# Optimization experiments

Hardware: AMD Instinct MI355X
Metric: run time of the kernel (lower is better)

The kernel has to match this reference:

```python
import jax, jax.numpy as jnp
import numpy as np

NUM_TAGS = 32            # init arg
N = NUM_TAGS + 2         # internal num_tags (start/end appended)
START = N - 2
END = N - 1
B = 1024
T = 1024
NEG = -6969.0            # module's 'minus infinity' constant


def setup_inputs() -> dict:
    key = jax.random.key(0)
    k1, k2 = jax.random.split(key)
    features = jax.random.normal(k1, (B, T, N), dtype=jnp.float32)
    # learned parameter: transition matrix [N, N]
    transitions = jax.random.normal(k2, (N, N), dtype=jnp.float32)
    return {"features": features, "transitions": transitions}


def _viterbi(features, transitions):
    # features: [B, T, N]; transitions: [N, N]
    Bn, Tn, Nn = features.shape
    init = jnp.full((Bn, Nn), NEG, dtype=features.dtype).at[:, START].set(0.0)

    def step(scores, feat):
        # score[b, j, k] = scores[b, k] + feat[b, j] + transitions[j, k]
        sc = scores[:, None, :] + feat[:, :, None] + transitions[None, :, :]
        return jnp.max(sc, axis=-1), jnp.argmax(sc, axis=-1)

    feats_t = jnp.swapaxes(features, 0, 1)            # [T, B, N]
    scores, paths = jax.lax.scan(step, init, feats_t)  # paths: [T, B, N] int

    scores = scores + transitions[END]                # add transition to end tag
    best = jnp.max(scores, axis=-1)                   # [B]
    idx = jnp.argmax(scores, axis=-1)                 # [B]

    # backtrack through backpointers, from t = T-1 down to 0
    def back(i, path):
        ni = jnp.take_along_axis(path, i[:, None], axis=1)[:, 0]
        return ni, ni

    _, tags = jax.lax.scan(back, idx, paths, reverse=True)  # tags: [T, B]
    best_path = jnp.concatenate([tags.T, idx[:, None]], axis=1)  # [B, T+1]
    return best, best_path


def reference(features, transitions):
    return _viterbi(features, transitions)
```

## Files before the change

### kernel.cpp

```cpp
#include <hip/hip_runtime.h>
#include <stdint.h>

#define BB 1024
#define TT 1024
#define NN 34
#define NP 36
#define NB 2
#define TPB (NB * 136)
#define NEGV -6969.0f
#define PADV -1.0e30f

template<int C>
__device__ __forceinline__ int dpp_i(int x) {
    return __builtin_amdgcn_update_dpp(0, x, C, 0xF, 0xF, true);
}
template<int C>
__device__ __forceinline__ float dpp_f(float x) {
    return __int_as_float(dpp_i<C>(__float_as_int(x)));
}

__device__ __forceinline__ void lds_barrier() {
    asm volatile("s_waitcnt lgkmcnt(0)\n\ts_barrier" ::: "memory");
}

__global__ __launch_bounds__(TPB, 3) void viterbi_full(
        const float* __restrict__ feat,
        const float* __restrict__ trans,
        unsigned char* __restrict__ bpg,
        float* __restrict__ out)
{
    __shared__ float sbuf[2][NB][NP];
    __shared__ float fsb[NB][NN];
    __shared__ unsigned char Fm[NB][16][NN];
    __shared__ int Eb[NB][16];
    __shared__ int idxs[NB];

    const int tid = threadIdx.x;
    const int bl  = (tid >= 136) ? 1 : 0;
    const int r   = tid - bl * 136;
    const int j   = r >> 2;
    const int h   = r & 3;
    const int k0  = h * 9;
    const int bg  = blockIdx.x * NB + bl;

    for (int e = tid; e < 2 * NB * NP; e += TPB) {
        int kk = e % NP;
        ((float*)sbuf)[e] = (kk >= NN) ? PADV : ((kk == 32) ? 0.0f : NEGV);
    }

    float tr[9];
    int   kreg[9];
#pragma unroll
    for (int i = 0; i < 9; ++i) {
        int k = k0 + i;
        tr[i]   = (k < NN) ? trans[j * NN + k] : 0.0f;
        kreg[i] = k;
    }
    const float trE = (r < NN) ? trans[33 * NN + r] : 0.0f;

    const float* fp = feat + (size_t)bg * TT * NN + j;
    unsigned char* bpt = bpg + (size_t)bg * TT * NN + j;

    float fr0 = fp[0 * NN], fr1 = fp[1 * NN], fr2 = fp[2 * NN], fr3 = fp[3 * NN];

    float* const s0 = &sbuf[0][bl][0];
    float* const s1 = &sbuf[1][bl][0];

    __syncthreads();

    auto vstep = [&](const float* __restrict__ srd, float* __restrict__ swr,
                     float fv, unsigned char* bpw) {
        float vv[9];
#pragma unroll
        for (int i = 0; i < 9; ++i) vv[i] = (srd[k0 + i] + fv) + tr[i];
        float m = fmaxf(fmaxf(fmaxf(vv[0], vv[1]), fmaxf(vv[2], vv[3])),
                        fmaxf(fmaxf(vv[4], vv[5]), fmaxf(vv[6], vv[7])));
        m = fmaxf(m, vv[8]);
        m = fmaxf(m, dpp_f<0xB1>(m));
        m = fmaxf(m, dpp_f<0x4E>(m));
        int am = 127;
#pragma unroll
        for (int i = 8; i >= 0; --i) am = (vv[i] == m) ? kreg[i] : am;
        int ao = dpp_i<0xB1>(am); am = (ao < am) ? ao : am;
        ao = dpp_i<0x4E>(am);     am = (ao < am) ? ao : am;
        if (h == 0) { swr[j] = m; *bpw = (unsigned char)am; }
        lds_barrier();
    };

    for (int n = 0; n < 255; ++n) {
        { float f = fr0; fr0 = fp[4 * NN]; vstep(s0, s1, f, bpt + 0 * NN); }
        { float f = fr1; fr1 = fp[5 * NN]; vstep(s1, s0, f, bpt + 1 * NN); }
        { float f = fr2; fr2 = fp[6 * NN]; vstep(s0, s1, f, bpt + 2 * NN); }
        { float f = fr3; fr3 = fp[7 * NN]; vstep(s1, s0, f, bpt + 3 * NN); }
        fp += 4 * NN; bpt += 4 * NN;
    }
    vstep(s0, s1, fr0, bpt + 0 * NN);
    vstep(s1, s0, fr1, bpt + 1 * NN);
    vstep(s0, s1, fr2, bpt + 2 * NN);
    vstep(s1, s0, fr3, bpt + 3 * NN);

    if (r < NN) fsb[bl][r] = s0[r] + trE;
    __syncthreads();
    if (r == 0) {
        float bm = fsb[bl][0]; int bi = 0;
        for (int k = 1; k < NN; ++k) {
            float v = fsb[bl][k];
            if (v > bm) { bm = v; bi = k; }
        }
        out[bg] = bm; idxs[bl] = bi;
    }
    __syncthreads();

    const unsigned char* __restrict__ bb = bpg + (size_t)bg * TT * NN;

    {
        int g = (r >= 102) ? 3 : ((r >= 68) ? 2 : ((r >= 34) ? 1 : 0));
        int x = r - 34 * g;
        int c0 = g, c1 = g + 4, c2 = g + 8, c3 = g + 12;
        int m0 = x, m1 = x, m2 = x, m3 = x;
        for (int i = 63; i >= 0; --i) {
            m0 = bb[(size_t)((c0 * 64 + i) * NN) + m0];
            m1 = bb[(size_t)((c1 * 64 + i) * NN) + m1];
            m2 = bb[(size_t)((c2 * 64 + i) * NN) + m2];
            m3 = bb[(size_t)((c3 * 64 + i) * NN) + m3];
        }
        Fm[bl][c0][x] = m0; Fm[bl][c1][x] = m1;
        Fm[bl][c2][x] = m2; Fm[bl][c3][x] = m3;
    }
    __syncthreads();

    if (r == 0) {
        int e = idxs[bl];
        Eb[bl][15] = e;
        for (int c = 15; c >= 1; --c) { e = Fm[bl][c][e]; Eb[bl][c - 1] = e; }
    }
    __syncthreads();

    float* po = out + BB + (size_t)bg * (TT + 1);
    if (r < 16) {
        int c = r;
        int m = Eb[bl][c];
        for (int i = 63; i >= 0; --i) {
            m = bb[(size_t)((c * 64 + i) * NN) + m];
            po[c * 64 + i] = (float)m;
        }
    }
    if (r == 16) po[TT] = (float)idxs[bl];
}

extern "C" void kernel_launch(void* const* d_in, const int* in_sizes, int n_in,
                              void* d_out, int out_size, void* d_ws, size_t ws_size,
                              hipStream_t stream) {
    const float* feat  = (const float*)d_in[0];
    const float* trans = (const float*)d_in[1];
    float* out = (float*)d_out;
    unsigned char* bp = (unsigned char*)d_ws;

    viterbi_full<<<BB / NB, TPB, 0, stream>>>(feat, trans, bp, out);
}
```

Baseline: 547.5 us.

## Run each sequence in one wavefront with register-resident scores and LDS backpointers

```diff
diff --git a/kernel.cpp b/kernel.cpp
--- a/kernel.cpp
+++ b/kernel.cpp
@@ -4,148 +4,130 @@
 #define BB 1024
 #define TT 1024
 #define NN 34
-#define NP 36
-#define NB 2
-#define TPB (NB * 136)
 #define NEGV -6969.0f
-#define PADV -1.0e30f
 
-template<int C>
-__device__ __forceinline__ int dpp_i(int x) {
-    return __builtin_amdgcn_update_dpp(0, x, C, 0xF, 0xF, true);
-}
-template<int C>
-__device__ __forceinline__ float dpp_f(float x) {
-    return __int_as_float(dpp_i<C>(__float_as_int(x)));
+__device__ __forceinline__ float rdlane_f(float v, int l) {
+    return __int_as_float(__builtin_amdgcn_readlane(__float_as_int(v), l));
 }
 
-__device__ __forceinline__ void lds_barrier() {
-    asm volatile("s_waitcnt lgkmcnt(0)\n\ts_barrier" ::: "memory");
-}
-
-__global__ __launch_bounds__(TPB, 3) void viterbi_full(
+__global__ __launch_bounds__(64) void viterbi_wave(
         const float* __restrict__ feat,
         const float* __restrict__ trans,
-        unsigned char* __restrict__ bpg,
         float* __restrict__ out)
 {
-    __shared__ float sbuf[2][NB][NP];
-    __shared__ float fsb[NB][NN];
-    __shared__ unsigned char Fm[NB][16][NN];
-    __shared__ int Eb[NB][16];
-    __shared__ int idxs[NB];
+    __shared__ unsigned char bp[TT * NN];
+    __shared__ unsigned char Fm[16 * NN];
 
-    const int tid = threadIdx.x;
-    const int bl  = (tid >= 136) ? 1 : 0;
-    const int r   = tid - bl * 136;
-    const int j   = r >> 2;
-    const int h   = r & 3;
-    const int k0  = h * 9;
-    const int bg  = blockIdx.x * NB + bl;
+    const int lane = threadIdx.x;
+    const int bg   = blockIdx.x;
+    const int jc   = (lane < NN) ? lane : (NN - 1);
 
-    for (int e = tid; e < 2 * NB * NP; e += TPB) {
-        int kk = e % NP;
-        ((float*)sbuf)[e] = (kk >= NN) ? PADV : ((kk == 32) ? 0.0f : NEGV);
-    }
+    float tr[NN];
+#pragma unroll
+    for (int k = 0; k < NN; ++k) tr[k] = trans[jc * NN + k];
+    const float trE = trans[33 * NN + jc];
 
-    float tr[9];
-    int   kreg[9];
-#pragma unroll
-    for (int i = 0; i < 9; ++i) {
-        int k = k0 + i;
-        tr[i]   = (k < NN) ? trans[j * NN + k] : 0.0f;
-        kreg[i] = k;
-    }
-    const float trE = (r < NN) ? trans[33 * NN + r] : 0.0f;
-
-    const float* fp = feat + (size_t)bg * TT * NN + j;
-    unsigned char* bpt = bpg + (size_t)bg * TT * NN + j;
-
+    const float* fp = feat + (size_t)bg * TT * NN + jc;
     float fr0 = fp[0 * NN], fr1 = fp[1 * NN], fr2 = fp[2 * NN], fr3 = fp[3 * NN];
 
-    float* const s0 = &sbuf[0][bl][0];
-    float* const s1 = &sbuf[1][bl][0];
+    float sk[NN];
+#pragma unroll
+    for (int k = 0; k < NN; ++k) sk[k] = (k == 32) ? 0.0f : NEGV;
 
-    __syncthreads();
+    float m = NEGV;
+    int tbase = 0;
 
-    auto vstep = [&](const float* __restrict__ srd, float* __restrict__ swr,
-                     float fv, unsigned char* bpw) {
-        float vv[9];
+    auto vstep = [&](float f) {
+        float vv[NN];
 #pragma unroll
-        for (int i = 0; i < 9; ++i) vv[i] = (srd[k0 + i] + fv) + tr[i];
-        float m = fmaxf(fmaxf(fmaxf(vv[0], vv[1]), fmaxf(vv[2], vv[3])),
-                        fmaxf(fmaxf(vv[4], vv[5]), fmaxf(vv[6], vv[7])));
-        m = fmaxf(m, vv[8]);
-        m = fmaxf(m, dpp_f<0xB1>(m));
-        m = fmaxf(m, dpp_f<0x4E>(m));
-        int am = 127;
+        for (int k = 0; k < NN; ++k) vv[k] = (sk[k] + f) + tr[k];
+
+        float t0[17];
 #pragma unroll
-        for (int i = 8; i >= 0; --i) am = (vv[i] == m) ? kreg[i] : am;
-        int ao = dpp_i<0xB1>(am); am = (ao < am) ? ao : am;
-        ao = dpp_i<0x4E>(am);     am = (ao < am) ? ao : am;
-        if (h == 0) { swr[j] = m; *bpw = (unsigned char)am; }
-        lds_barrier();
+        for (int k = 0; k < 17; ++k) t0[k] = fmaxf(vv[2 * k], vv[2 * k + 1]);
+        float t1[8];
+#pragma unroll
+        for (int k = 0; k < 8; ++k) t1[k] = fmaxf(t0[2 * k], t0[2 * k + 1]);
+        float t2a = fmaxf(fmaxf(t1[0], t1[1]), fmaxf(t1[2], t1[3]));
+        float t2b = fmaxf(fmaxf(t1[4], t1[5]), fmaxf(t1[6], t1[7]));
+        float mx  = fmaxf(fmaxf(t2a, t2b), t0[16]);
+
+        int am0 = 127, am1 = 127, am2 = 127, am3 = 127;
+#pragma unroll
+        for (int k = NN - 1; k >= 0; --k) {
+            bool e = (vv[k] == mx);
+            if ((k & 3) == 0) am0 = e ? k : am0;
+            else if ((k & 3) == 1) am1 = e ? k : am1;
+            else if ((k & 3) == 2) am2 = e ? k : am2;
+            else am3 = e ? k : am3;
+        }
+        int am = min(min(am0, am1), min(am2, am3));
+
+        if (lane < NN) bp[tbase + lane] = (unsigned char)am;
+        tbase += NN;
+
+#pragma unroll
+        for (int k = 0; k < NN; ++k) sk[k] = rdlane_f(mx, k);
+        m = mx;
     };
 
     for (int n = 0; n < 255; ++n) {
-        { float f = fr0; fr0 = fp[4 * NN]; vstep(s0, s1, f, bpt + 0 * NN); }
-        { float f = fr1; fr1 = fp[5 * NN]; vstep(s1, s0, f, bpt + 1 * NN); }
-        { float f = fr2; fr2 = fp[6 * NN]; vstep(s0, s1, f, bpt + 2 * NN); }
-        { float f = fr3; fr3 = fp[7 * NN]; vstep(s1, s0, f, bpt + 3 * NN); }
-        fp += 4 * NN; bpt += 4 * NN;
+        { float f = fr0; fr0 = fp[4 * NN]; vstep(f); }
+        { float f = fr1; fr1 = fp[5 * NN]; vstep(f); }
+        { float f = fr2; fr2 = fp[6 * NN]; vstep(f); }
+        { float f = fr3; fr3 = fp[7 * NN]; vstep(f); }
+        fp += 4 * NN;
     }
-    vstep(s0, s1, fr0, bpt + 0 * NN);
-    vstep(s1, s0, fr1, bpt + 1 * NN);
-    vstep(s0, s1, fr2, bpt + 2 * NN);
-    vstep(s1, s0, fr3, bpt + 3 * NN);
+    vstep(fr0); vstep(fr1); vstep(fr2); vstep(fr3);
 
-    if (r < NN) fsb[bl][r] = s0[r] + trE;
-    __syncthreads();
-    if (r == 0) {
-        float bm = fsb[bl][0]; int bi = 0;
-        for (int k = 1; k < NN; ++k) {
-            float v = fsb[bl][k];
-            if (v > bm) { bm = v; bi = k; }
-        }
-        out[bg] = bm; idxs[bl] = bi;
+    float fs = m + trE;
+    float bm = rdlane_f(fs, 0);
+    int bi = 0;
+#pragma unroll
+    for (int k = 1; k < NN; ++k) {
+        float v = rdlane_f(fs, k);
+        bool g = (v > bm);
+        bm = g ? v : bm;
+        bi = g ? k : bi;
     }
-    __syncthreads();
+    if (lane == 0) out[bg] = bm;
 
-    const unsigned char* __restrict__ bb = bpg + (size_t)bg * TT * NN;
+    int cc[9], xx[9], mm[9], cb[9];
+#pragma unroll
+    for (int r = 0; r < 9; ++r) {
+        int job = 64 * r + lane;
+        if (job > 543) job = 543;
+        cc[r] = job / 34;
+        xx[r] = job - 34 * cc[r];
+        mm[r] = xx[r];
+        cb[r] = cc[r] * (64 * NN);
+    }
+    for (int i = 63; i >= 0; --i) {
+        int ib = i * NN;
+#pragma unroll
+        for (int r = 0; r < 9; ++r) mm[r] = bp[cb[r] + ib + mm[r]];
+    }
+#pragma unroll
+    for (int r = 0; r < 9; ++r) Fm[cc[r] * NN + xx[r]] = (unsigned char)mm[r];
 
-    {
-        int g = (r >= 102) ? 3 : ((r >= 68) ? 2 : ((r >= 34) ? 1 : 0));
-        int x = r - 34 * g;
-        int c0 = g, c1 = g + 4, c2 = g + 8, c3 = g + 12;
-        int m0 = x, m1 = x, m2 = x, m3 = x;
-        for (int i = 63; i >= 0; --i) {
-            m0 = bb[(size_t)((c0 * 64 + i) * NN) + m0];
-            m1 = bb[(size_t)((c1 * 64 + i) * NN) + m1];
-            m2 = bb[(size_t)((c2 * 64 + i) * NN) + m2];
-            m3 = bb[(size_t)((c3 * 64 + i) * NN) + m3];
-        }
-        Fm[bl][c0][x] = m0; Fm[bl][c1][x] = m1;
-        Fm[bl][c2][x] = m2; Fm[bl][c3][x] = m3;
+    int e = bi;
+    int myeb = (lane == 15) ? e : 0;
+#pragma unroll
+    for (int c2 = 15; c2 >= 1; --c2) {
+        e = Fm[c2 * NN + e];
+        myeb = (lane == c2 - 1) ? e : myeb;
     }
-    __syncthreads();
-
-    if (r == 0) {
-        int e = idxs[bl];
-        Eb[bl][15] = e;
-        for (int c = 15; c >= 1; --c) { e = Fm[bl][c][e]; Eb[bl][c - 1] = e; }
-    }
-    __syncthreads();
 
     float* po = out + BB + (size_t)bg * (TT + 1);
-    if (r < 16) {
-        int c = r;
-        int m = Eb[bl][c];
+    if (lane < 16) {
+        int mm2 = myeb;
+        int base = lane * (64 * NN);
         for (int i = 63; i >= 0; --i) {
-            m = bb[(size_t)((c * 64 + i) * NN) + m];
-            po[c * 64 + i] = (float)m;
+            mm2 = bp[base + i * NN + mm2];
+            po[lane * 64 + i] = (float)mm2;
         }
     }
-    if (r == 16) po[TT] = (float)idxs[bl];
+    if (lane == 16) po[TT] = (float)bi;
 }
 
 extern "C" void kernel_launch(void* const* d_in, const int* in_sizes, int n_in,
@@ -154,7 +136,6 @@
     const float* feat  = (const float*)d_in[0];
     const float* trans = (const float*)d_in[1];
     float* out = (float*)d_out;
-    unsigned char* bp = (unsigned char*)d_ws;
 
-    viterbi_full<<<BB / NB, TPB, 0, stream>>>(feat, trans, bp, out);
+    viterbi_wave<<<BB, 64, 0, stream>>>(feat, trans, out);
 }
```

New measurement: 674.2 us. +23.2%, slower.
